# Optimization experiments

Hardware: AMD Instinct MI355X
Metric: run time of the kernel (lower is better)

The kernel has to match this reference:

```python
import jax, jax.numpy as jnp
import numpy as np

B, N, D, E, HEADS, HID = 8, 2048, 768, 4, 12, 3072
CAPF = 0.25
CAP = int(CAPF * N)  # 512 tokens per expert
DH = D // HEADS
EPS = 1e-5  # torch LayerNorm default
SCALE = 0.02


def _nested_masks(dim, n_exp):
    # expert e keeps the first dim // 2**e features (nested experts, MoNE)
    m = np.zeros((n_exp, dim), np.float32)
    for e in range(n_exp):
        m[e, : dim >> e] = 1.0
    return jnp.asarray(m)


def _ln(x, g, b):
    mu = x.mean(-1, keepdims=True)
    var = ((x - mu) ** 2).mean(-1, keepdims=True)
    return (x - mu) * jax.lax.rsqrt(var + EPS) * g + b


def setup_inputs() -> dict:
    key = jax.random.key(0)
    ks = jax.random.split(key, 8)
    return {
        "x": jax.random.normal(ks[0], (B, N, D), jnp.float32),
        "Wr": jax.random.normal(ks[1], (D, E), jnp.float32) * SCALE,
        "ln1_g": jnp.ones((D,), jnp.float32),
        "ln1_b": jnp.zeros((D,), jnp.float32),
        "ln2_g": jnp.ones((D,), jnp.float32),
        "ln2_b": jnp.zeros((D,), jnp.float32),
        "Wqkv": jax.random.normal(ks[2], (D, 3 * D), jnp.float32) * SCALE,
        "Wproj": jax.random.normal(ks[3], (D, D), jnp.float32) * SCALE,
        "bproj": jnp.zeros((D,), jnp.float32),
        "W1": jax.random.normal(ks[4], (D, HID), jnp.float32) * SCALE,
        "b1": jnp.zeros((HID,), jnp.float32),
        "W2": jax.random.normal(ks[5], (HID, D), jnp.float32) * SCALE,
        "b2": jnp.zeros((D,), jnp.float32),
    }


def reference(x, Wr, ln1_g, ln1_b, ln2_g, ln2_b, Wqkv, Wproj, bproj, W1, b1, W2, b2):
    mD = _nested_masks(D, E)[None, :, None, :]    # [1,E,1,D]
    mH = _nested_masks(HID, E)[None, :, None, :]  # [1,E,1,HID]

    # ---- expert-choice router ----
    probs = jax.nn.softmax(x @ Wr, axis=-1)                     # [B,N,E]
    gates, idx = jax.lax.top_k(probs.transpose(0, 2, 1), CAP)   # each [B,E,C]
    dispatch = jax.nn.one_hot(idx, N, dtype=x.dtype)            # [B,E,C,N]
    combine = dispatch * gates[..., None]                       # [B,E,C,N]

    # ---- attention branch (per-expert nested-masked attention) ----
    xn = _ln(x, ln1_g, ln1_b)
    xe = jnp.einsum('becn,bnd->becd', dispatch, xn)             # [B,E,C,D]
    qkv = (xe * mD) @ Wqkv                                      # input-masked linear
    q, k, v = jnp.split(qkv, 3, axis=-1)
    q, k, v = q * mD, k * mD, v * mD                            # nested output masks

    def to_heads(t):
        return t.reshape(B, E, CAP, HEADS, DH).transpose(0, 1, 3, 2, 4)  # [B,E,H,C,dh]

    q, k, v = to_heads(q), to_heads(k), to_heads(v)
    att = jax.nn.softmax(jnp.einsum('behcd,behkd->behck', q, k) * (DH ** -0.5), axis=-1)
    o = jnp.einsum('behck,behkd->behcd', att, v)
    o = o.transpose(0, 1, 3, 2, 4).reshape(B, E, CAP, D)
    ye = ((o @ Wproj) + bproj) * mD                             # masked proj
    x = x + jnp.einsum('becd,becn->bnd', ye, combine)           # combine back

    # ---- MLP branch (per-expert nested-masked MLP) ----
    xn2 = _ln(x, ln2_g, ln2_b)
    xe2 = jnp.einsum('becn,bnd->becd', dispatch, xn2)           # [B,E,C,D]
    h = jax.nn.gelu((((xe2 * mD) @ W1) + b1) * mH)              # [B,E,C,HID]
    y = ((h @ W2) + b2) * mD                                    # [B,E,C,D]
    x = x + jnp.einsum('becd,becn->bnd', y, combine)
    return x
```

## Files before the change

### kernel.cpp

```cpp
#include <hip/hip_runtime.h>
#include <stdint.h>

typedef uint16_t u16;
typedef uint32_t u32;
typedef uint64_t u64;
typedef float f32x4 __attribute__((ext_vector_type(4)));
typedef __bf16 bf16x8 __attribute__((ext_vector_type(8)));

#define DEVI __device__ __forceinline__

struct U4 { u32 a, b, c, d; };

DEVI u16 f2bf(float f) {
    u32 u = __builtin_bit_cast(u32, f);
    return (u16)((u + 0x7FFFu + ((u >> 16) & 1u)) >> 16);
}
DEVI float bf2f(u32 h) { return __builtin_bit_cast(float, h << 16); }
DEVI u32 cvt_pk_bf16(float lo, float hi) {
    u32 r;
    asm("v_cvt_pk_bf16_f32 %0, %1, %2" : "=v"(r) : "v"(lo), "v"(hi));
    return r;
}

DEVI float gelu_f(float x) {
    float u = 0.7978845608028654f * (x + 0.044715f * x * x * x);
    float t = exp2f(u * 2.885390081777927f);
    return x * (1.f - 1.f / (t + 1.f));
}

#define GLOAD_LDS16(gp, lp) \
    __builtin_amdgcn_global_load_lds((const __attribute__((address_space(1))) void*)(gp), \
                                     (__attribute__((address_space(3))) void*)(lp), 16, 0, 0)

struct WtJobs {
    const float* src[4]; u16* dst[4];
    int K[4], N[4], ntx[4], start[5];
};
__global__ __launch_bounds__(256) void wt_all_kernel(WtJobs a) {
    int j = 0;
#pragma unroll
    for (int k = 1; k < 4; k++) if ((int)blockIdx.x >= a.start[k]) j = k;
    const int local = blockIdx.x - a.start[j];
    const int N = a.N[j], K = a.K[j];
    const int n0 = (local % a.ntx[j]) * 32, k0 = (local / a.ntx[j]) * 32;
    const float* __restrict__ src = a.src[j];
    u16* __restrict__ dst = a.dst[j];
    __shared__ float tile[32][33];
    int tx = threadIdx.x & 31, ty = threadIdx.x >> 5;
#pragma unroll
    for (int i = 0; i < 32; i += 8)
        tile[ty + i][tx] = src[(size_t)(k0 + ty + i) * N + n0 + tx];
    __syncthreads();
#pragma unroll
    for (int i = 0; i < 32; i += 8)
        dst[(size_t)(n0 + ty + i) * K + k0 + tx] = f2bf(tile[tx][ty + i]);
}

__global__ __launch_bounds__(256) void routerln_kernel(const float* __restrict__ x,
                                                       const float* __restrict__ Wr,
                                                       const float* __restrict__ gw,
                                                       const float* __restrict__ bw,
                                                       float* __restrict__ probs,
                                                       u16* __restrict__ xn) {
    int wv = threadIdx.x >> 6, lane = threadIdx.x & 63;
    size_t t = (size_t)blockIdx.x * 4 + wv;
    const float4* xr = (const float4*)(x + t * 768);
    const float4* wr4 = (const float4*)Wr;
    float4 v[3]; float s = 0, s2 = 0, a0 = 0, a1 = 0, a2 = 0, a3 = 0;
#pragma unroll
    for (int i = 0; i < 3; i++) {
        int f4 = lane + 64 * i;
        v[i] = xr[f4];
        s += v[i].x + v[i].y + v[i].z + v[i].w;
        s2 += v[i].x * v[i].x + v[i].y * v[i].y + v[i].z * v[i].z + v[i].w * v[i].w;
#pragma unroll
        for (int jj = 0; jj < 4; jj++) {
            float xv = (jj == 0) ? v[i].x : (jj == 1) ? v[i].y : (jj == 2) ? v[i].z : v[i].w;
            float4 w = wr4[f4 * 4 + jj];
            a0 = fmaf(xv, w.x, a0); a1 = fmaf(xv, w.y, a1);
            a2 = fmaf(xv, w.z, a2); a3 = fmaf(xv, w.w, a3);
        }
    }
#pragma unroll
    for (int m = 1; m < 64; m <<= 1) {
        s += __shfl_xor(s, m); s2 += __shfl_xor(s2, m);
        a0 += __shfl_xor(a0, m); a1 += __shfl_xor(a1, m);
        a2 += __shfl_xor(a2, m); a3 += __shfl_xor(a3, m);
    }
    float mx = fmaxf(fmaxf(a0, a1), fmaxf(a2, a3));
    float e0 = expf(a0 - mx), e1 = expf(a1 - mx), e2 = expf(a2 - mx), e3 = expf(a3 - mx);
    float inv = 1.f / (e0 + e1 + e2 + e3);
    if (lane < 4) {
        float pv = (lane == 0) ? e0 : (lane == 1) ? e1 : (lane == 2) ? e2 : e3;
        int b = (int)(t >> 11), n = (int)(t & 2047);
        probs[(size_t)(b * 4 + lane) * 2048 + n] = pv * inv;
    }
    float mu = s * (1.f / 768.f);
    float var = s2 * (1.f / 768.f) - mu * mu;
    float rs = rsqrtf(var + 1e-5f);
    uint2* op = (uint2*)(xn + t * 768);
#pragma unroll
    for (int i = 0; i < 3; i++) {
        int j4 = (lane + 64 * i) * 4;
        float y0 = (v[i].x - mu) * rs * gw[j4 + 0] + bw[j4 + 0];
        float y1 = (v[i].y - mu) * rs * gw[j4 + 1] + bw[j4 + 1];
        float y2 = (v[i].z - mu) * rs * gw[j4 + 2] + bw[j4 + 2];
        float y3 = (v[i].w - mu) * rs * gw[j4 + 3] + bw[j4 + 3];
        uint2 o; o.x = cvt_pk_bf16(y0, y1); o.y = cvt_pk_bf16(y2, y3);
        op[lane + 64 * i] = o;
    }
}

__global__ __launch_bounds__(1024) void topk_kernel(const float* __restrict__ probs,
                                                    int* __restrict__ idx, float* __restrict__ gate,
                                                    int* __restrict__ rev) {
    int be = blockIdx.x; int b = be >> 2, e = be & 3;
    __shared__ u64 keys[2048];
    for (int n = threadIdx.x; n < 2048; n += 1024) {
        u32 p = __builtin_bit_cast(u32, probs[(size_t)be * 2048 + n]);
        keys[n] = ((u64)p << 32) | (u32)(2047 - n);
        rev[((size_t)b * 2048 + n) * 4 + e] = -1;
    }
    __syncthreads();
    for (int k = 2; k <= 2048; k <<= 1)
        for (int j = k >> 1; j > 0; j >>= 1) {
            for (int i = threadIdx.x; i < 2048; i += 1024) {
                int ixj = i ^ j;
                if (ixj > i) {
                    u64 a = keys[i], bb = keys[ixj];
                    bool up = ((i & k) == 0);
                    if (up ? (a < bb) : (a > bb)) { keys[i] = bb; keys[ixj] = a; }
                }
            }
            __syncthreads();
        }
    for (int c = threadIdx.x; c < 512; c += 1024) {
        u64 kk = keys[c];
        int n = 2047 - (int)(kk & 0xffffffffu);
        idx[be * 512 + c] = n;
        gate[be * 512 + c] = __builtin_bit_cast(float, (u32)(kk >> 32));
        rev[((size_t)b * 2048 + n) * 4 + e] = c;
    }
}

struct GemmJobs {
    const u16* A[4]; u16* C[4]; u16* VT[4]; const int* idx[4];
    const u16* BT; const float* bias;
    long sAb[4], sCb[4], sVb[4];
    int lda[4], ldc[4], nk[4], nmask[4], tps[4], tstart[4];
    int ldb;
};

template <int MODE>
__global__ __launch_bounds__(256) void gemm_kernel(GemmJobs a) {
    __shared__ __align__(16) char smem[2][16384];
    const int tid = threadIdx.x, wv = tid >> 6, lane = tid & 63;
    const int bid = blockIdx.x;
    const int bz = bid & 7;
    const int mt = (bid >> 3) & 3;
    const int sidx = bid >> 5;
    int e = 0;
#pragma unroll
    for (int k = 1; k < 4; k++) if (sidx >= a.tstart[k]) e = k;
    const int local = sidx - a.tstart[e];
    int seg, ntl;
    if (MODE == 0) { seg = local / a.tps[e]; ntl = local - seg * a.tps[e]; }
    else { seg = 0; ntl = local; }
    const int nbase = seg * 768 + ntl * 128;
    const int lda = a.lda[e], ldc = a.ldc[e], nk = a.nk[e], nmask = a.nmask[e];
    const u16* Ap = a.A[e] + (long)bz * a.sAb[e];
    const int* ix = a.idx[e] ? (a.idx[e] + bz * 2048) : nullptr;
    const bool swapped = (MODE != 0) || (seg < 2);

    auto stage = [&](int buf, int kt) {
        char* base = smem[buf] + ((wv >= 2) ? 8192 : 0);
        const int kb = kt * 32;
#pragma unroll
        for (int q = 0; q < 4; q++) {
            int i8 = (wv & 1) * 4 + q;
            int row = i8 * 16 + (lane >> 2);
            int clog = ((lane & 3) * 16) ^ ((row & 6) << 3);
            const u16* g;
            if (wv < 2) {
                int rs = ix ? ix[mt * 128 + row] : (mt * 128 + row);
                g = Ap + (long)rs * lda + kb;
            } else {
                g = a.BT + (long)(nbase + row) * a.ldb + kb;
            }
            GLOAD_LDS16((const char*)g + clog, base + i8 * 1024);
        }
    };

    f32x4 acc[4][4] = {};
    stage(0, 0);
    __syncthreads();
    int buf = 0;
    const int wr = wv >> 1, wc = wv & 1;
    const int l15 = lane & 15, lg = lane >> 4;
    const int cb = lg * 16;
    for (int kt = 0; kt < nk; kt++) {
        if (kt + 1 < nk) stage(buf ^ 1, kt + 1);
        const char* ab = smem[buf];
        const char* bb = smem[buf] + 8192;
        bf16x8 af[4], bfv[4];
#pragma unroll
        for (int mi = 0; mi < 4; mi++) {
            int r = wr * 64 + mi * 16 + l15;
            af[mi] = *(const bf16x8*)(ab + r * 64 + (cb ^ ((r & 6) << 3)));
        }
#pragma unroll
        for (int ni = 0; ni < 4; ni++) {
            int r = wc * 64 + ni * 16 + l15;
            bfv[ni] = *(const bf16x8*)(bb + r * 64 + (cb ^ ((r & 6) << 3)));
        }
        __builtin_amdgcn_s_setprio(1);
        if (swapped) {
#pragma unroll
            for (int mi = 0; mi < 4; mi++)
#pragma unroll
                for (int ni = 0; ni < 4; ni++)
                    acc[mi][ni] = __builtin_amdgcn_mfma_f32_16x16x32_bf16(bfv[ni], af[mi], acc[mi][ni], 0, 0, 0);
        } else {
#pragma unroll
            for (int mi = 0; mi < 4; mi++)
#pragma unroll
                for (int ni = 0; ni < 4; ni++)
                    acc[mi][ni] = __builtin_amdgcn_mfma_f32_16x16x32_bf16(af[mi], bfv[ni], acc[mi][ni], 0, 0, 0);
        }
        __builtin_amdgcn_s_setprio(0);
        __syncthreads();
        buf ^= 1;
    }

    u16* Cb = a.C[e] + (long)bz * a.sCb[e];
    if (MODE == 0 && seg == 2) {
        u16* Vb = a.VT[e] + (long)bz * a.sVb[e];
#pragma unroll
        for (int mi = 0; mi < 4; mi++) {
            const int r0 = mt * 128 + wr * 64 + mi * 16 + (lg << 2);
#pragma unroll
            for (int ni = 0; ni < 4; ni++) {
                const int nloc = ntl * 128 + wc * 64 + ni * 16 + l15;
                const bool act = nloc < nmask;
                uint2 pv;
                if (act) { pv.x = cvt_pk_bf16(acc[mi][ni][0], acc[mi][ni][1]);
                           pv.y = cvt_pk_bf16(acc[mi][ni][2], acc[mi][ni][3]); }
                else { pv.x = 0; pv.y = 0; }
                *(uint2*)(Vb + (long)nloc * 512 + r0) = pv;
            }
        }
    } else if (MODE == 0) {
#pragma unroll
        for (int mi = 0; mi < 4; mi++) {
            const int row = mt * 128 + wr * 64 + mi * 16 + l15;
            u16* cp = Cb + (long)row * 1536 + seg * 768 + ntl * 128;
#pragma unroll
            for (int ni = 0; ni < 4; ni++) {
                const int colb = wc * 64 + ni * 16 + lg * 4;
                const bool act = (ntl * 128 + colb) < nmask;
                uint2 pv;
                if (act) { pv.x = cvt_pk_bf16(acc[mi][ni][0], acc[mi][ni][1]);
                           pv.y = cvt_pk_bf16(acc[mi][ni][2], acc[mi][ni][3]); }
                else { pv.x = 0; pv.y = 0; }
                *(uint2*)(cp + colb) = pv;
            }
        }
    } else {
#pragma unroll
        for (int mi = 0; mi < 4; mi++) {
            const int row = mt * 128 + wr * 64 + mi * 16 + l15;
#pragma unroll
            for (int ni = 0; ni < 4; ni++) {
                const int nloc = ntl * 128 + wc * 64 + ni * 16 + lg * 4;
                const float4 bv = *(const float4*)(a.bias + nloc);
                float v0 = acc[mi][ni][0] + bv.x, v1 = acc[mi][ni][1] + bv.y;
                float v2 = acc[mi][ni][2] + bv.z, v3 = acc[mi][ni][3] + bv.w;
                if (MODE == 2) { v0 = gelu_f(v0); v1 = gelu_f(v1); v2 = gelu_f(v2); v3 = gelu_f(v3); }
                uint2 pv; pv.x = cvt_pk_bf16(v0, v1); pv.y = cvt_pk_bf16(v2, v3);
                *(uint2*)(Cb + (long)row * ldc + nloc) = pv;
            }
        }
    }
}

__global__ __launch_bounds__(256) void attn_kernel(const u16* __restrict__ qkv,
                                                   const u16* __restrict__ vt,
                                                   u16* __restrict__ obuf) {
    const int bid = blockIdx.x;
    const int jobl = bid % 184;
    const int qt = bid / 184;
    const int b = jobl / 23, hj = jobl % 23;
    int e, h;
    if (hj < 12) { e = 0; h = hj; }
    else if (hj < 18) { e = 1; h = hj - 12; }
    else if (hj < 21) { e = 2; h = hj - 18; }
    else { e = 3; h = hj - 21; }
    const int job = b * 4 + e;
    const u16* qkvj = qkv + (size_t)job * 512 * 1536;
    const u16* vtj = vt + (size_t)job * 768 * 512 + (size_t)h * 64 * 512;
    u16* oj = obuf + (size_t)job * 512 * 768;
    __shared__ __align__(16) char lds[32768];
    char* Klds = lds;
    char* Vlds = lds + 16384;
    const int tid = threadIdx.x, wv = tid >> 6;
    const int lane = tid & 63, l15 = lane & 15, lg = lane >> 4;
    const int q0 = qt * 128 + wv * 32;

    bf16x8 qf[2][2];
#pragma unroll
    for (int n2 = 0; n2 < 2; n2++)
#pragma unroll
        for (int ks = 0; ks < 2; ks++)
            qf[n2][ks] = *(const bf16x8*)(qkvj + (size_t)(q0 + n2 * 16 + l15) * 1536 + h * 64 + ks * 32 + lg * 8);

    uint4 kreg[4], vreg[4];
    const int fr = tid >> 3, fch = tid & 7;
    const int fdl = tid >> 4, fcv = tid & 15;
    auto issue = [&](int t) {
        const int kv0 = t * 128;
#pragma unroll
        for (int ii = 0; ii < 4; ii++) {
            kreg[ii] = *(const uint4*)(qkvj + (size_t)(kv0 + fr + 32 * ii) * 1536 + 768 + h * 64 + fch * 8);
            vreg[ii] = *(const uint4*)(vtj + (size_t)(fdl + 16 * ii) * 512 + kv0 + fcv * 8);
        }
    };

    f32x4 oacc[4][2] = {};
    float mrun[2] = {-1e30f, -1e30f}, lrun[2] = {0.f, 0.f};
    const float SA = 0.18033688011112042f;

    issue(0);
    for (int t = 0; t < 4; t++) {
        __syncthreads();
#pragma unroll
        for (int ii = 0; ii < 4; ii++) {
            int r = fr + 32 * ii;
            *(uint4*)(Klds + r * 128 + ((fch * 16) ^ ((r & 7) << 4))) = kreg[ii];
            int dl = fdl + 16 * ii;
            *(uint4*)(Vlds + dl * 256 + ((fcv * 16) ^ ((dl & 7) << 4))) = vreg[ii];
        }
        __syncthreads();
        if (t < 3) issue(t + 1);

        f32x4 sacc[8][2] = {};
        __builtin_amdgcn_s_setprio(1);
#pragma unroll
        for (int ks = 0; ks < 2; ks++)
#pragma unroll
            for (int m8 = 0; m8 < 8; m8++) {
                int r = m8 * 16 + l15;
                bf16x8 kf = *(const bf16x8*)(Klds + r * 128 + ((ks * 64 + lg * 16) ^ ((r & 7) << 4)));
#pragma unroll
                for (int n2 = 0; n2 < 2; n2++)
                    sacc[m8][n2] = __builtin_amdgcn_mfma_f32_16x16x32_bf16(kf, qf[n2][ks], sacc[m8][n2], 0, 0, 0);
            }
        __builtin_amdgcn_s_setprio(0);

        u32 pk[8][2][2];
#pragma unroll
        for (int n2 = 0; n2 < 2; n2++) {
            float pm[8];
#pragma unroll
            for (int m8 = 0; m8 < 8; m8++)
                pm[m8] = fmaxf(fmaxf(sacc[m8][n2][0], sacc[m8][n2][1]),
                               fmaxf(sacc[m8][n2][2], sacc[m8][n2][3]));
            float tm = fmaxf(fmaxf(fmaxf(pm[0], pm[1]), fmaxf(pm[2], pm[3])),
                             fmaxf(fmaxf(pm[4], pm[5]), fmaxf(pm[6], pm[7])));
            tm = fmaxf(tm, __shfl_xor(tm, 16));
            tm = fmaxf(tm, __shfl_xor(tm, 32));
            float mnew = fmaxf(mrun[n2], tm);
            float alpha = exp2f((mrun[n2] - mnew) * SA);
            float ps[8];
#pragma unroll
            for (int m8 = 0; m8 < 8; m8++) {
#pragma unroll
                for (int j = 0; j < 4; j++)
                    sacc[m8][n2][j] = exp2f((sacc[m8][n2][j] - mnew) * SA);
                ps[m8] = (sacc[m8][n2][0] + sacc[m8][n2][1]) + (sacc[m8][n2][2] + sacc[m8][n2][3]);
            }
            float tsum = ((ps[0] + ps[1]) + (ps[2] + ps[3])) + ((ps[4] + ps[5]) + (ps[6] + ps[7]));
            tsum += __shfl_xor(tsum, 16);
            tsum += __shfl_xor(tsum, 32);
            lrun[n2] = lrun[n2] * alpha + tsum;
            mrun[n2] = mnew;
#pragma unroll
            for (int mo = 0; mo < 4; mo++) oacc[mo][n2] *= alpha;
#pragma unroll
            for (int m8 = 0; m8 < 8; m8++) {
                pk[m8][n2][0] = cvt_pk_bf16(sacc[m8][n2][0], sacc[m8][n2][1]);
                pk[m8][n2][1] = cvt_pk_bf16(sacc[m8][n2][2], sacc[m8][n2][3]);
            }
        }

        const int la = ((2 * lg) & 3) * 16 + l15;
        const int lb = ((2 * lg + 1) & 3) * 16 + l15;
#pragma unroll
        for (int kb = 0; kb < 4; kb++) {
            bf16x8 pb[2];
#pragma unroll
            for (int n2 = 0; n2 < 2; n2++) {
                u32 w[4];
#pragma unroll
                for (int half = 0; half < 2; half++) {
                    int src = (half == 0) ? la : lb;
                    u32 aA = (u32)__shfl((int)pk[2 * kb + 0][n2][0], src);
                    u32 aB = (u32)__shfl((int)pk[2 * kb + 1][n2][0], src);
                    u32 bA = (u32)__shfl((int)pk[2 * kb + 0][n2][1], src);
                    u32 bB = (u32)__shfl((int)pk[2 * kb + 1][n2][1], src);
                    w[half * 2 + 0] = (lg < 2) ? aA : aB;
                    w[half * 2 + 1] = (lg < 2) ? bA : bB;
                }
                U4 uw{w[0], w[1], w[2], w[3]};
                pb[n2] = __builtin_bit_cast(bf16x8, uw);
            }
            __builtin_amdgcn_s_setprio(1);
#pragma unroll
            for (int mo = 0; mo < 4; mo++) {
                int r = mo * 16 + l15;
                bf16x8 vf = *(const bf16x8*)(Vlds + r * 256 + ((kb * 64 + lg * 16) ^ ((r & 7) << 4)));
#pragma unroll
                for (int n2 = 0; n2 < 2; n2++)
                    oacc[mo][n2] = __builtin_amdgcn_mfma_f32_16x16x32_bf16(vf, pb[n2], oacc[mo][n2], 0, 0, 0);
            }
            __builtin_amdgcn_s_setprio(0);
        }
    }

    __syncthreads();
    char* Wl = lds + wv * 4096;
#pragma unroll
    for (int n2 = 0; n2 < 2; n2++) {
        float inv = 1.f / lrun[n2];
        int c = n2 * 16 + l15;
#pragma unroll
        for (int mo = 0; mo < 4; mo++) {
            int tch = mo * 2 + (lg >> 1);
            int byteoff = c * 128 + (((tch ^ (c & 7)) << 4)) + (lg & 1) * 8;
            uint2 o;
            o.x = cvt_pk_bf16(oacc[mo][n2][0] * inv, oacc[mo][n2][1] * inv);
            o.y = cvt_pk_bf16(oacc[mo][n2][2] * inv, oacc[mo][n2][3] * inv);
            *(uint2*)(Wl + byteoff) = o;
        }
    }
    asm volatile("s_waitcnt lgkmcnt(0)" ::: "memory");
    __builtin_amdgcn_sched_barrier(0);
#pragma unroll
    for (int p = 0; p < 4; p++) {
        int row = p * 8 + (lane >> 3);
        int tch = lane & 7;
        uint4 v = *(const uint4*)(Wl + row * 128 + ((tch ^ (row & 7)) << 4));
        *(uint4*)(oj + (size_t)(q0 + row) * 768 + h * 64 + tch * 8) = v;
    }
}

template <int DO_LN>
__global__ __launch_bounds__(256) void combineln_kernel(const float* __restrict__ basex,
                                                        float* __restrict__ outp,
                                                        const u16* __restrict__ ye,
                                                        const int* __restrict__ rev,
                                                        const float* __restrict__ gate,
                                                        const float* __restrict__ gw,
                                                        const float* __restrict__ bw,
                                                        u16* __restrict__ xn) {
    int wv = threadIdx.x >> 6, lane = threadIdx.x & 63;
    size_t t = (size_t)blockIdx.x * 4 + wv;
    const int b = (int)(t >> 11);
    const int4 rv = *(const int4*)(rev + t * 4);
    const int cs[4] = {rv.x, rv.y, rv.z, rv.w};
    float4 v[3];
#pragma unroll
    for (int i = 0; i < 3; i++) v[i] = *(const float4*)(basex + t * 768 + (lane + 64 * i) * 4);
#pragma unroll
    for (int e = 0; e < 4; e++) {
        const int c = cs[e];
        if (c >= 0) {
            const int job = b * 4 + e;
            const float g = gate[job * 512 + c];
            const u16* yr = ye + ((size_t)job * 512 + c) * 768;
#pragma unroll
            for (int i = 0; i < 3; i++) {
                int f4 = lane + 64 * i;
                if (f4 < (192 >> e)) {
                    uint2 raw = *(const uint2*)(yr + f4 * 4);
                    v[i].x += g * bf2f(raw.x & 0xffffu);
                    v[i].y += g * bf2f(raw.x >> 16);
                    v[i].z += g * bf2f(raw.y & 0xffffu);
                    v[i].w += g * bf2f(raw.y >> 16);
                }
            }
        }
    }
#pragma unroll
    for (int i = 0; i < 3; i++) *(float4*)(outp + t * 768 + (lane + 64 * i) * 4) = v[i];
    if (DO_LN) {
        float s = 0, s2 = 0;
#pragma unroll
        for (int i = 0; i < 3; i++) {
            s += v[i].x + v[i].y + v[i].z + v[i].w;
            s2 += v[i].x * v[i].x + v[i].y * v[i].y + v[i].z * v[i].z + v[i].w * v[i].w;
        }
#pragma unroll
        for (int m = 1; m < 64; m <<= 1) { s += __shfl_xor(s, m); s2 += __shfl_xor(s2, m); }
        float mu = s * (1.f / 768.f);
        float var = s2 * (1.f / 768.f) - mu * mu;
        float rs = rsqrtf(var + 1e-5f);
        uint2* op = (uint2*)(xn + t * 768);
#pragma unroll
        for (int i = 0; i < 3; i++) {
            int j4 = (lane + 64 * i) * 4;
            float y0 = (v[i].x - mu) * rs * gw[j4 + 0] + bw[j4 + 0];
            float y1 = (v[i].y - mu) * rs * gw[j4 + 1] + bw[j4 + 1];
            float y2 = (v[i].z - mu) * rs * gw[j4 + 2] + bw[j4 + 2];
            float y3 = (v[i].w - mu) * rs * gw[j4 + 3] + bw[j4 + 3];
            uint2 o; o.x = cvt_pk_bf16(y0, y1); o.y = cvt_pk_bf16(y2, y3);
            op[lane + 64 * i] = o;
        }
    }
}

extern "C" void kernel_launch(void* const* d_in, const int* in_sizes, int n_in,
                              void* d_out, int out_size, void* d_ws, size_t ws_size,
                              hipStream_t stream) {
    (void)in_sizes; (void)n_in; (void)out_size; (void)ws_size;
    const float* x     = (const float*)d_in[0];
    const float* Wr    = (const float*)d_in[1];
    const float* ln1g  = (const float*)d_in[2];
    const float* ln1b  = (const float*)d_in[3];
    const float* ln2g  = (const float*)d_in[4];
    const float* ln2b  = (const float*)d_in[5];
    const float* Wqkv  = (const float*)d_in[6];
    const float* Wproj = (const float*)d_in[7];
    const float* bproj = (const float*)d_in[8];
    const float* W1    = (const float*)d_in[9];
    const float* b1    = (const float*)d_in[10];
    const float* W2    = (const float*)d_in[11];
    const float* b2    = (const float*)d_in[12];
    float* outp = (float*)d_out;

    char* ws = (char*)d_ws;
    size_t off = 0;
    auto take = [&](size_t bytes) -> void* {
        void* p = ws + off;
        off += (bytes + 255) & ~(size_t)255;
        return p;
    };
    u16*   WqkvT  = (u16*)take((size_t)2304 * 768 * 2);
    u16*   WprojT = (u16*)take((size_t)768 * 768 * 2);
    u16*   W1T    = (u16*)take((size_t)3072 * 768 * 2);
    u16*   W2T    = (u16*)take((size_t)768 * 3072 * 2);
    float* probs  = (float*)take((size_t)32 * 2048 * 4);
    int*   idxb   = (int*)take((size_t)32 * 512 * 4);
    float* gateb  = (float*)take((size_t)32 * 512 * 4);
    int*   revb   = (int*)take((size_t)8 * 2048 * 4 * 4);
    u16*   xn     = (u16*)take((size_t)8 * 2048 * 768 * 2);
    u16*   qkvb   = (u16*)take((size_t)32 * 512 * 1536 * 2);
    u16*   vtb    = (u16*)take((size_t)32 * 768 * 512 * 2);
    u16*   ob     = (u16*)take((size_t)32 * 512 * 768 * 2);
    u16*   yeb    = (u16*)take((size_t)32 * 512 * 768 * 2);
    u16*   hb     = qkvb;

    const int Dk_[4] = {768, 384, 192, 96};
    const int He_[4] = {3072, 1536, 768, 384};
    size_t eoffH[4];
    { size_t s = 0; for (int e = 0; e < 4; e++) { eoffH[e] = s; s += (size_t)8 * 512 * He_[e]; } }

    WtJobs wj{};
    wj.src[0] = Wqkv;  wj.dst[0] = WqkvT;  wj.K[0] = 768;  wj.N[0] = 2304;
    wj.src[1] = Wproj; wj.dst[1] = WprojT; wj.K[1] = 768;  wj.N[1] = 768;
    wj.src[2] = W1;    wj.dst[2] = W1T;    wj.K[2] = 768;  wj.N[2] = 3072;
    wj.src[3] = W2;    wj.dst[3] = W2T;    wj.K[3] = 3072; wj.N[3] = 768;
    { int s = 0; for (int j = 0; j < 4; j++) { wj.ntx[j] = wj.N[j] / 32; wj.start[j] = s; s += (wj.N[j] / 32) * (wj.K[j] / 32); } wj.start[4] = s;
      wt_all_kernel<<<s, 256, 0, stream>>>(wj); }

    routerln_kernel<<<4096, 256, 0, stream>>>(x, Wr, ln1g, ln1b, probs, xn);
    topk_kernel<<<32, 1024, 0, stream>>>(probs, idxb, gateb, revb);

    {
        GemmJobs ga{};
        ga.BT = WqkvT; ga.bias = nullptr; ga.ldb = 768;
        int s = 0;
        for (int e = 0; e < 4; e++) {
            int tps = (Dk_[e] + 127) / 128;
            ga.A[e] = xn; ga.C[e] = qkvb + (size_t)e * 512 * 1536; ga.VT[e] = vtb + (size_t)e * 768 * 512;
            ga.idx[e] = idxb + e * 512;
            ga.sAb[e] = (long)2048 * 768; ga.sCb[e] = (long)4 * 512 * 1536; ga.sVb[e] = (long)4 * 768 * 512;
            ga.lda[e] = 768; ga.ldc[e] = 1536; ga.nk[e] = Dk_[e] / 32; ga.nmask[e] = Dk_[e];
            ga.tps[e] = tps; ga.tstart[e] = s; s += 3 * tps;
        }
        gemm_kernel<0><<<s * 32, 256, 0, stream>>>(ga);
    }

    attn_kernel<<<736, 256, 0, stream>>>(qkvb, vtb, ob);

    {
        GemmJobs ga{};
        ga.BT = WprojT; ga.bias = bproj; ga.ldb = 768;
        int s = 0;
        for (int e = 0; e < 4; e++) {
            int tps = (Dk_[e] + 127) / 128;
            ga.A[e] = ob + (size_t)e * 512 * 768; ga.C[e] = yeb + (size_t)e * 512 * 768;
            ga.VT[e] = nullptr; ga.idx[e] = nullptr;
            ga.sAb[e] = (long)4 * 512 * 768; ga.sCb[e] = (long)4 * 512 * 768; ga.sVb[e] = 0;
            ga.lda[e] = 768; ga.ldc[e] = 768; ga.nk[e] = Dk_[e] / 32; ga.nmask[e] = 768;
            ga.tps[e] = tps; ga.tstart[e] = s; s += tps;
        }
        gemm_kernel<1><<<s * 32, 256, 0, stream>>>(ga);
    }

    combineln_kernel<1><<<4096, 256, 0, stream>>>(x, outp, yeb, revb, gateb, ln2g, ln2b, xn);

    {
        GemmJobs ga{};
        ga.BT = W1T; ga.bias = b1; ga.ldb = 768;
        int s = 0;
        for (int e = 0; e < 4; e++) {
            ga.A[e] = xn; ga.C[e] = hb + eoffH[e]; ga.VT[e] = nullptr; ga.idx[e] = idxb + e * 512;
            ga.sAb[e] = (long)2048 * 768; ga.sCb[e] = (long)512 * He_[e]; ga.sVb[e] = 0;
            ga.lda[e] = 768; ga.ldc[e] = He_[e]; ga.nk[e] = Dk_[e] / 32; ga.nmask[e] = He_[e];
            ga.tps[e] = He_[e] / 128; ga.tstart[e] = s; s += He_[e] / 128;
        }
        gemm_kernel<2><<<s * 32, 256, 0, stream>>>(ga);
    }
    {
        GemmJobs ga{};
        ga.BT = W2T; ga.bias = b2; ga.ldb = 3072;
        int s = 0;
        for (int e = 0; e < 4; e++) {
            int tps = (Dk_[e] + 127) / 128;
            ga.A[e] = hb + eoffH[e]; ga.C[e] = yeb + (size_t)e * 512 * 768;
            ga.VT[e] = nullptr; ga.idx[e] = nullptr;
            ga.sAb[e] = (long)512 * He_[e]; ga.sCb[e] = (long)4 * 512 * 768; ga.sVb[e] = 0;
            ga.lda[e] = He_[e]; ga.ldc[e] = 768; ga.nk[e] = He_[e] / 32; ga.nmask[e] = 768;
            ga.tps[e] = tps; ga.tstart[e] = s; s += tps;
        }
        gemm_kernel<1><<<s * 32, 256, 0, stream>>>(ga);
    }

    combineln_kernel<0><<<4096, 256, 0, stream>>>(outp, outp, yeb, revb, gateb, nullptr, nullptr, nullptr);
}
```

Before: 498.3 us.

## Load attention K/V fragments directly from global memory instead of LDS staging

The attention kernel no longer stages K and V tiles through shared memory with register prefetch and barriers. Each wave now reads its MFMA K and V fragments straight from global memory, relying on L1/L2 caching. LDS shrinks to the output staging buffer, and the s_setprio hints are dropped in both the GEMM and attention kernels. This removes the barriers and LDS traffic, but the four waves now issue redundant global loads of the same K/V data and lose the software prefetch overlap.

Measured after the change: 509.7 us. 2.3% more time.

```diff
diff --git a/kernel.cpp b/kernel.cpp
--- a/kernel.cpp
+++ b/kernel.cpp
@@ -213,7 +213,6 @@
             int r = wc * 64 + ni * 16 + l15;
             bfv[ni] = *(const bf16x8*)(bb + r * 64 + (cb ^ ((r & 6) << 3)));
         }
-        __builtin_amdgcn_s_setprio(1);
         if (swapped) {
 #pragma unroll
             for (int mi = 0; mi < 4; mi++)
@@ -227,7 +226,6 @@
                 for (int ni = 0; ni < 4; ni++)
                     acc[mi][ni] = __builtin_amdgcn_mfma_f32_16x16x32_bf16(af[mi], bfv[ni], acc[mi][ni], 0, 0, 0);
         }
-        __builtin_amdgcn_s_setprio(0);
         __syncthreads();
         buf ^= 1;
     }
@@ -299,9 +297,7 @@
     const u16* qkvj = qkv + (size_t)job * 512 * 1536;
     const u16* vtj = vt + (size_t)job * 768 * 512 + (size_t)h * 64 * 512;
     u16* oj = obuf + (size_t)job * 512 * 768;
-    __shared__ __align__(16) char lds[32768];
-    char* Klds = lds;
-    char* Vlds = lds + 16384;
+    __shared__ __align__(16) char lds[16384];
     const int tid = threadIdx.x, wv = tid >> 6;
     const int lane = tid & 63, l15 = lane & 15, lg = lane >> 4;
     const int q0 = qt * 128 + wv * 32;
@@ -313,48 +309,23 @@
         for (int ks = 0; ks < 2; ks++)
             qf[n2][ks] = *(const bf16x8*)(qkvj + (size_t)(q0 + n2 * 16 + l15) * 1536 + h * 64 + ks * 32 + lg * 8);
 
-    uint4 kreg[4], vreg[4];
-    const int fr = tid >> 3, fch = tid & 7;
-    const int fdl = tid >> 4, fcv = tid & 15;
-    auto issue = [&](int t) {
-        const int kv0 = t * 128;
-#pragma unroll
-        for (int ii = 0; ii < 4; ii++) {
-            kreg[ii] = *(const uint4*)(qkvj + (size_t)(kv0 + fr + 32 * ii) * 1536 + 768 + h * 64 + fch * 8);
-            vreg[ii] = *(const uint4*)(vtj + (size_t)(fdl + 16 * ii) * 512 + kv0 + fcv * 8);
-        }
-    };
-
     f32x4 oacc[4][2] = {};
     float mrun[2] = {-1e30f, -1e30f}, lrun[2] = {0.f, 0.f};
     const float SA = 0.18033688011112042f;
 
-    issue(0);
     for (int t = 0; t < 4; t++) {
-        __syncthreads();
-#pragma unroll
-        for (int ii = 0; ii < 4; ii++) {
-            int r = fr + 32 * ii;
-            *(uint4*)(Klds + r * 128 + ((fch * 16) ^ ((r & 7) << 4))) = kreg[ii];
-            int dl = fdl + 16 * ii;
-            *(uint4*)(Vlds + dl * 256 + ((fcv * 16) ^ ((dl & 7) << 4))) = vreg[ii];
-        }
-        __syncthreads();
-        if (t < 3) issue(t + 1);
+        const int kv0 = t * 128;
 
         f32x4 sacc[8][2] = {};
-        __builtin_amdgcn_s_setprio(1);
 #pragma unroll
         for (int ks = 0; ks < 2; ks++)
 #pragma unroll
             for (int m8 = 0; m8 < 8; m8++) {
-                int r = m8 * 16 + l15;
-                bf16x8 kf = *(const bf16x8*)(Klds + r * 128 + ((ks * 64 + lg * 16) ^ ((r & 7) << 4)));
+                bf16x8 kf = *(const bf16x8*)(qkvj + (size_t)(kv0 + m8 * 16 + l15) * 1536 + 768 + h * 64 + ks * 32 + lg * 8);
 #pragma unroll
                 for (int n2 = 0; n2 < 2; n2++)
                     sacc[m8][n2] = __builtin_amdgcn_mfma_f32_16x16x32_bf16(kf, qf[n2][ks], sacc[m8][n2], 0, 0, 0);
             }
-        __builtin_amdgcn_s_setprio(0);
 
         u32 pk[8][2][2];
 #pragma unroll
@@ -413,20 +384,16 @@
                 U4 uw{w[0], w[1], w[2], w[3]};
                 pb[n2] = __builtin_bit_cast(bf16x8, uw);
             }
-            __builtin_amdgcn_s_setprio(1);
 #pragma unroll
             for (int mo = 0; mo < 4; mo++) {
-                int r = mo * 16 + l15;
-                bf16x8 vf = *(const bf16x8*)(Vlds + r * 256 + ((kb * 64 + lg * 16) ^ ((r & 7) << 4)));
+                bf16x8 vf = *(const bf16x8*)(vtj + (size_t)(mo * 16 + l15) * 512 + kv0 + kb * 32 + lg * 8);
 #pragma unroll
                 for (int n2 = 0; n2 < 2; n2++)
                     oacc[mo][n2] = __builtin_amdgcn_mfma_f32_16x16x32_bf16(vf, pb[n2], oacc[mo][n2], 0, 0, 0);
             }
-            __builtin_amdgcn_s_setprio(0);
-        }
-    }
-
-    __syncthreads();
+        }
+    }
+
     char* Wl = lds + wv * 4096;
 #pragma unroll
     for (int n2 = 0; n2 < 2; n2++) {
```
